# Kernel tuning notes

Hardware: AMD Instinct MI355X
Metric: run time of the kernel (lower is better)

## Reference

```python
import jax, jax.numpy as jnp
import numpy as np

B, H, W, D = 8, 64, 64, 512
NH, DK = 16, 32
WS, SH = 8, 4            # window size, shift size = WS // 2
L = 4                    # n_layer
WS2 = WS * WS
NWH, NWW = H // WS, W // WS
SCALE = 1.0 / np.sqrt(DK)


def _rel_index(ws):
    # standard Swin relative position index: (ws^2, ws^2) into a (2ws-1)^2 table
    coords = np.stack(np.meshgrid(np.arange(ws), np.arange(ws), indexing='ij'))
    cf = coords.reshape(2, -1)
    rel = cf[:, :, None] - cf[:, None, :] + (ws - 1)
    return (rel[0] * (2 * ws - 1) + rel[1]).astype(np.int32)


def _shift_mask():
    # Swin-style shifted-window attention mask for cyclic shift by SH
    img = np.zeros((H, W), dtype=np.int32)
    cnt = 0
    sls = (slice(0, -WS), slice(-WS, -SH), slice(-SH, None))
    for hs in sls:
        for ws_ in sls:
            img[hs, ws_] = cnt
            cnt += 1
    win = img.reshape(NWH, WS, NWW, WS).transpose(0, 2, 1, 3).reshape(NWH, NWW, WS2)
    m = win[..., None, :] != win[..., :, None]          # (nh, nw, ws2, ws2)
    return np.broadcast_to(m[None, None], (1, NH, NWH, NWW, WS2, WS2)).copy()


def setup_inputs() -> dict:
    key = jax.random.key(0)
    ks = jax.random.split(key, 12)
    s = 0.02
    inp = {
        'x': jax.random.normal(ks[0], (B, H, W, D), jnp.float32),
        'mask': jnp.asarray(_shift_mask()),
        'rel_index': jnp.asarray(_rel_index(WS)),
        'Wq': jax.random.normal(ks[1], (L, D, D), jnp.float32) * s,
        'bq': jnp.zeros((L, D), jnp.float32),
        'Wkv': jax.random.normal(ks[2], (L, D, 2 * D), jnp.float32) * s,
        'bkv': jnp.zeros((L, 2 * D), jnp.float32),
        'Wo': jax.random.normal(ks[3], (L, D, D), jnp.float32) * s,
        'bo': jnp.zeros((L, D), jnp.float32),
        'rel_table': jax.random.normal(ks[4], (L, (2 * WS - 1) ** 2, NH), jnp.float32) * s,
        'ln1_g': jnp.ones((L, D), jnp.float32),
        'ln1_b': jnp.zeros((L, D), jnp.float32),
        'ln2_g': jnp.ones((L, D), jnp.float32),
        'ln2_b': jnp.zeros((L, D), jnp.float32),
        'W1': jax.random.normal(ks[5], (L, D, 4 * D), jnp.float32) * s,
        'b1': jnp.zeros((L, 4 * D), jnp.float32),
        'W2': jax.random.normal(ks[6], (L, 4 * D, D), jnp.float32) * s,
        'b2': jnp.zeros((L, D), jnp.float32),
    }
    return inp


def _ln(x, g, b):
    m = jnp.mean(x, -1, keepdims=True)
    v = jnp.mean(jnp.square(x - m), -1, keepdims=True)
    return (x - m) * jax.lax.rsqrt(v + 1e-5) * g + b


def _partition(t):
    # (B,H,W,NH,DK) -> (B,NH,nh,nw,ws^2,DK)
    t = t.reshape(B, NWH, WS, NWW, WS, NH, DK)
    return t.transpose(0, 5, 1, 3, 2, 4, 6).reshape(B, NH, NWH, NWW, WS2, DK)


def _merge(t):
    # (B,NH,nh,nw,ws^2,DK) -> (B,H,W,NH,DK)
    t = t.reshape(B, NH, NWH, NWW, WS, WS, DK).transpose(0, 2, 4, 3, 5, 1, 6)
    return t.reshape(B, H, W, NH, DK)


def _attn(xn, mask, rel_index, Wq, bq, Wkv, bkv, Wo, bo, table):
    q = (xn @ Wq + bq).reshape(B, H, W, NH, DK)
    kv = (xn @ Wkv + bkv).reshape(B, H, W, 2, NH, DK)
    k, v = kv[..., 0, :, :], kv[..., 1, :, :]
    # cyclic shift (shifting=True since n_class=4)
    q = jnp.roll(q, (-SH, -SH), axis=(1, 2))
    k = jnp.roll(k, (-SH, -SH), axis=(1, 2))
    v = jnp.roll(v, (-SH, -SH), axis=(1, 2))
    qw, kw, vw = _partition(q), _partition(k), _partition(v)
    scores = jnp.einsum('bhnmqd,bhnmkd->bhnmqk', qw, kw) * SCALE
    bias = table[rel_index]                      # (ws2, ws2, NH)
    scores = scores + bias.transpose(2, 0, 1)[None, :, None, None]
    scores = jnp.where(mask, -1e9, scores)
    a = jax.nn.softmax(scores, axis=-1)
    o = jnp.einsum('bhnmqk,bhnmkd->bhnmqd', a, vw)
    o = _merge(o)
    o = jnp.roll(o, (SH, SH), axis=(1, 2))       # reverse cyclic shift
    return o.reshape(B, H, W, D) @ Wo + bo


def reference(x, mask, rel_index, Wq, bq, Wkv, bkv, Wo, bo, rel_table,
              ln1_g, ln1_b, ln2_g, ln2_b, W1, b1, W2, b2):
    for i in range(L):
        x = x + _attn(_ln(x, ln1_g[i], ln1_b[i]), mask, rel_index,
                      Wq[i], bq[i], Wkv[i], bkv[i], Wo[i], bo[i], rel_table[i])
        h = _ln(x, ln2_g[i], ln2_b[i])
        x = x + (jax.nn.gelu(h @ W1[i] + b1[i]) @ W2[i] + b2[i])
    return x
```

## Files before the change

### kernel.cpp

```cpp
#include <hip/hip_runtime.h>
#include <hip/hip_bf16.h>

typedef __hip_bfloat16 bf16;
typedef __attribute__((ext_vector_type(8))) short short8;
typedef __attribute__((ext_vector_type(4))) float f32x4;

#define GLDS16(g, l) __builtin_amdgcn_global_load_lds(                              \
    (__attribute__((address_space(1))) const void*)(g),                             \
    (__attribute__((address_space(3))) void*)(l), 16, 0, 0)

#define SCALE_ 0.17677669529663687f

__global__ void detect_k(const unsigned int* __restrict__ ln1g_raw, int* __restrict__ flag)
{
    if (threadIdx.x == 0) *flag = (ln1g_raw[0] == 0x3F803F80u) ? 0 : 1;
}

__global__ __launch_bounds__(256)
void cvt_small_k(const void* __restrict__ src, bf16* __restrict__ dst, const int n,
                 const int* __restrict__ flag)
{
    const int i = blockIdx.x * 256 + threadIdx.x;
    if (i >= n) return;
    const bool f32 = (*flag != 0);
    dst[i] = f32 ? (bf16)((const float*)src)[i] : ((const bf16*)src)[i];
}

__global__ void transpose2_k(const float* __restrict__ inF, const bf16* __restrict__ inB,
                             bf16* __restrict__ out, const int R, const int C,
                             const int* __restrict__ flag)
{
    __shared__ bf16 tile[32][33];
    const bool f32 = (*flag != 0);
    const int c0 = blockIdx.x * 32, r0 = blockIdx.y * 32;
    const int tx = threadIdx.x, ty = threadIdx.y;
#pragma unroll
    for (int k = 0; k < 4; k++) {
        const long idx = (long)(r0 + ty + k * 8) * C + c0 + tx;
        tile[ty + k * 8][tx] = f32 ? (bf16)inF[idx] : inB[idx];
    }
    __syncthreads();
#pragma unroll
    for (int k = 0; k < 4; k++)
        out[(long)(c0 + ty + k * 8) * R + r0 + tx] = tile[tx][ty + k * 8];
}

__device__ __forceinline__ float gelu_f(float v)
{
    const float u = 0.7978845608028654f * (v + 0.044715f * v * v * v);
    const float e = __expf(-2.0f * u);
    return v * __builtin_amdgcn_rcpf(1.0f + e);
}

#define SBAR()   __builtin_amdgcn_s_barrier()
#define SCHED0() __builtin_amdgcn_sched_barrier(0)
#define WLGKM()  { asm volatile("s_waitcnt lgkmcnt(0)"); SCHED0(); }

template <int EPI>
__global__ __launch_bounds__(512, 2)
void gemm256(const bf16* __restrict__ A, const bf16* __restrict__ Bt,
             const bf16* __restrict__ bias0, const bf16* __restrict__ bias1,
             const int split,
             bf16* __restrict__ outb, float* __restrict__ outf,
             float* __restrict__ outf2,
             const int M, const int N, const int K)
{
    __shared__ char smem[131072] __attribute__((aligned(16)));

    const int nT  = N >> 8;
    const int nwg = gridDim.x;
    const int bid = blockIdx.x;
    const int wg = (bid & 7) * (nwg >> 3) + (bid >> 3);
    const int mb = wg / nT;
    const int nb = wg - mb * nT;
    const int m0 = mb << 8, n0 = nb << 8;

    const int tid  = threadIdx.x;
    const int lane = tid & 63;
    const int wave = tid >> 6;
    const int wm = wave >> 2;
    const int wn = wave & 3;
    const int fr  = lane & 15;
    const int oct = lane >> 4;
    const int l8  = lane >> 3;
    const int cx  = (lane & 7) ^ l8;

    const int T = K >> 6;

    const bf16* Asrc = A  + (long)(m0 + wm * 128 + wn * 32 + l8) * K + cx * 8;
    char*       Adst = smem + wm * 16384 + wn * 4096;
    const int h    = wn >> 1;
    const int bsub = wm * 2 + (wn & 1);
    const bf16* Bsrc = Bt + (long)(n0 + h * 128 + bsub * 32 + l8) * K + cx * 8;
    char*       Bdst = smem + 65536 + h * 16384 + bsub * 4096;

#define STAGE_A(kt, p) {                                                   \
        const bf16* s_ = Asrc + (long)(kt) * 64;                           \
        char* d_ = Adst + (p) * 32768;                                     \
        GLDS16(s_,            d_);                                         \
        GLDS16(s_ +  8L * K,  d_ + 1024);                                  \
        GLDS16(s_ + 16L * K,  d_ + 2048);                                  \
        GLDS16(s_ + 24L * K,  d_ + 3072); }
#define STAGE_B(kt, p) {                                                   \
        const bf16* s_ = Bsrc + (long)(kt) * 64;                           \
        char* d_ = Bdst + (p) * 32768;                                     \
        GLDS16(s_,            d_);                                         \
        GLDS16(s_ +  8L * K,  d_ + 1024);                                  \
        GLDS16(s_ + 16L * K,  d_ + 2048);                                  \
        GLDS16(s_ + 24L * K,  d_ + 3072); }

    const int kx0 = (     oct * 16) ^ ((fr & 7) << 4);
    const int kx1 = (64 + oct * 16) ^ ((fr & 7) << 4);
    const int aoff = (wm * 128 + fr) * 128;
    const int boff = 65536 + (wn * 64 + fr) * 128;

    f32x4 acc[8][4];
#pragma unroll
    for (int m = 0; m < 8; m++)
#pragma unroll
        for (int n = 0; n < 4; n++) acc[m][n] = (f32x4){0.f, 0.f, 0.f, 0.f};

    short8 af[4][2], bf[4][2];

    STAGE_B(0, 0); STAGE_A(0, 0);
    STAGE_B(1, 1); STAGE_A(1, 1);
    SCHED0();
    asm volatile("s_waitcnt vmcnt(8)");
    SCHED0();
    SBAR();

    for (int t = 0; t < T; ++t) {
        const int pOff = (t & 1) << 15;

#pragma unroll
        for (int mm = 0; mm < 4; mm++) {
            af[mm][0] = *(const short8*)(smem + pOff + aoff + mm * 2048 + kx0);
            af[mm][1] = *(const short8*)(smem + pOff + aoff + mm * 2048 + kx1);
        }
#pragma unroll
        for (int nn = 0; nn < 2; nn++) {
            bf[nn][0] = *(const short8*)(smem + pOff + boff + nn * 2048 + kx0);
            bf[nn][1] = *(const short8*)(smem + pOff + boff + nn * 2048 + kx1);
        }
        SCHED0();
        SBAR();
        WLGKM();
        __builtin_amdgcn_s_setprio(1);
#pragma unroll
        for (int ks = 0; ks < 2; ks++)
#pragma unroll
            for (int mm = 0; mm < 4; mm++)
#pragma unroll
                for (int nn = 0; nn < 2; nn++)
                    acc[mm][nn] = __builtin_amdgcn_mfma_f32_16x16x32_bf16(
                        bf[nn][ks], af[mm][ks], acc[mm][nn], 0, 0, 0);
        __builtin_amdgcn_s_setprio(0);
        SCHED0();
        SBAR();

#pragma unroll
        for (int nn = 2; nn < 4; nn++) {
            bf[nn][0] = *(const short8*)(smem + pOff + boff + nn * 2048 + kx0);
            bf[nn][1] = *(const short8*)(smem + pOff + boff + nn * 2048 + kx1);
        }
        SCHED0();
        SBAR();
        WLGKM();
        __builtin_amdgcn_s_setprio(1);
#pragma unroll
        for (int ks = 0; ks < 2; ks++)
#pragma unroll
            for (int mm = 0; mm < 4; mm++)
#pragma unroll
                for (int nn = 2; nn < 4; nn++)
                    acc[mm][nn] = __builtin_amdgcn_mfma_f32_16x16x32_bf16(
                        bf[nn][ks], af[mm][ks], acc[mm][nn], 0, 0, 0);
        __builtin_amdgcn_s_setprio(0);
        SCHED0();
        SBAR();

#pragma unroll
        for (int mm = 0; mm < 4; mm++) {
            af[mm][0] = *(const short8*)(smem + pOff + aoff + (4 + mm) * 2048 + kx0);
            af[mm][1] = *(const short8*)(smem + pOff + aoff + (4 + mm) * 2048 + kx1);
        }
        SCHED0();
        if (t < T - 2) STAGE_B(t + 2, (t & 1));
        SCHED0();
        SBAR();
        WLGKM();
        __builtin_amdgcn_s_setprio(1);
#pragma unroll
        for (int ks = 0; ks < 2; ks++)
#pragma unroll
            for (int mm = 0; mm < 4; mm++)
#pragma unroll
                for (int nn = 2; nn < 4; nn++)
                    acc[4 + mm][nn] = __builtin_amdgcn_mfma_f32_16x16x32_bf16(
                        bf[nn][ks], af[mm][ks], acc[4 + mm][nn], 0, 0, 0);
        __builtin_amdgcn_s_setprio(0);
        SCHED0();
        SBAR();

        if (t < T - 2) STAGE_A(t + 2, (t & 1));
        SCHED0();
        __builtin_amdgcn_s_setprio(1);
#pragma unroll
        for (int ks = 0; ks < 2; ks++)
#pragma unroll
            for (int mm = 0; mm < 4; mm++)
#pragma unroll
                for (int nn = 0; nn < 2; nn++)
                    acc[4 + mm][nn] = __builtin_amdgcn_mfma_f32_16x16x32_bf16(
                        bf[nn][ks], af[mm][ks], acc[4 + mm][nn], 0, 0, 0);
        __builtin_amdgcn_s_setprio(0);
        SCHED0();
        if (t < T - 2)       { asm volatile("s_waitcnt vmcnt(8)"); }
        else if (t == T - 2) { asm volatile("s_waitcnt vmcnt(0)"); }
        SCHED0();
        SBAR();
    }
#undef STAGE_A
#undef STAGE_B

    if (EPI >= 2) {
        const int erow = m0 + wm * 128 + fr;
        const int ecol = n0 + wn * 64 + (oct << 2);
#pragma unroll
        for (int nn = 0; nn < 4; nn++) {
            const int col0 = ecol + nn * 16;
            const bf16* bp = (col0 < split) ? (bias0 + col0) : (bias1 + (col0 - split));
            const float bv0 = (float)bp[0], bv1 = (float)bp[1];
            const float bv2 = (float)bp[2], bv3 = (float)bp[3];
#pragma unroll
            for (int mm = 0; mm < 8; mm++) {
                const long base = (long)(erow + mm * 16) * N + col0;
                float4 o = *(const float4*)(outf + base);
                o.x += acc[mm][nn][0] + bv0;
                o.y += acc[mm][nn][1] + bv1;
                o.z += acc[mm][nn][2] + bv2;
                o.w += acc[mm][nn][3] + bv3;
                if (EPI == 2) *(float4*)(outf  + base) = o;
                else          *(float4*)(outf2 + base) = o;
            }
        }
    } else {
        const int col_l = wn * 64 + (oct << 2);
#pragma unroll
        for (int nn = 0; nn < 4; nn++) {
            const int cl = col_l + nn * 16;
            const int cg = n0 + cl;
            const bf16* bp = (cg < split) ? (bias0 + cg) : (bias1 + (cg - split));
            const float bv0 = (float)bp[0], bv1 = (float)bp[1];
            const float bv2 = (float)bp[2], bv3 = (float)bp[3];
#pragma unroll
            for (int mm = 0; mm < 8; mm++) {
                const int row_l = wm * 128 + mm * 16 + fr;
                float v0 = acc[mm][nn][0] + bv0;
                float v1 = acc[mm][nn][1] + bv1;
                float v2 = acc[mm][nn][2] + bv2;
                float v3 = acc[mm][nn][3] + bv3;
                if (EPI == 1) { v0 = gelu_f(v0); v1 = gelu_f(v1); v2 = gelu_f(v2); v3 = gelu_f(v3); }
                union { ushort4 u; bf16 hh[4]; } pk;
                pk.hh[0] = (bf16)v0; pk.hh[1] = (bf16)v1;
                pk.hh[2] = (bf16)v2; pk.hh[3] = (bf16)v3;
                int ad = (row_l << 9) + (cl << 1);
                ad ^= ((row_l & 7) << 4);
                *(ushort4*)(smem + ad) = pk.u;
            }
        }
        asm volatile("s_waitcnt lgkmcnt(0)");
        SBAR();
        const int rgrp = tid >> 5;
        const int chnk = tid & 31;
#pragma unroll
        for (int rr = 0; rr < 16; rr++) {
            const int row_l = rgrp * 16 + rr;
            int ad = (row_l << 9) + (chnk << 4);
            ad ^= ((row_l & 7) << 4);
            const uint4 val = *(const uint4*)(smem + ad);
            *(uint4*)((char*)outb + ((long)(m0 + row_l) * N + n0) * 2 + (chnk << 4)) = val;
        }
    }
}

__global__ __launch_bounds__(256)
void ln_k(const float* __restrict__ x, const bf16* __restrict__ g,
          const bf16* __restrict__ b, bf16* __restrict__ out)
{
    const int token = blockIdx.x * 4 + (threadIdx.x >> 6);
    const int lane  = threadIdx.x & 63;
    const float* xp = x + (long)token * 512 + lane * 8;
    float4 u0 = ((const float4*)xp)[0];
    float4 u1 = ((const float4*)xp)[1];
    float v[8] = {u0.x, u0.y, u0.z, u0.w, u1.x, u1.y, u1.z, u1.w};
    float s = 0.f, ss = 0.f;
#pragma unroll
    for (int e = 0; e < 8; e++) { s += v[e]; ss += v[e] * v[e]; }
#pragma unroll
    for (int off = 1; off < 64; off <<= 1) {
        s  += __shfl_xor(s,  off);
        ss += __shfl_xor(ss, off);
    }
    const float mean = s * (1.0f / 512.0f);
    const float var  = ss * (1.0f / 512.0f) - mean * mean;
    const float rstd = rsqrtf(var + 1e-5f);
    union { uint4 u; bf16 h[8]; } gg, bb, oo;
    gg.u = *(const uint4*)(g + lane * 8);
    bb.u = *(const uint4*)(b + lane * 8);
#pragma unroll
    for (int e = 0; e < 8; e++)
        oo.h[e] = (bf16)((v[e] - mean) * rstd * (float)gg.h[e] + (float)bb.h[e]);
    *(uint4*)(out + (long)token * 512 + lane * 8) = oo.u;
}

__global__ __launch_bounds__(256)
void lnx_k(const void* __restrict__ xin, const bf16* __restrict__ g,
           const bf16* __restrict__ b, float* __restrict__ xf,
           bf16* __restrict__ out, const int* __restrict__ flag)
{
    const int token = blockIdx.x * 4 + (threadIdx.x >> 6);
    const int lane  = threadIdx.x & 63;
    float v[8];
    if (*flag != 0) {
        const float* xp = (const float*)xin + (long)token * 512 + lane * 8;
        float4 u0 = ((const float4*)xp)[0];
        float4 u1 = ((const float4*)xp)[1];
        v[0] = u0.x; v[1] = u0.y; v[2] = u0.z; v[3] = u0.w;
        v[4] = u1.x; v[5] = u1.y; v[6] = u1.z; v[7] = u1.w;
    } else {
        union { uint4 u; bf16 h[8]; } t;
        t.u = *(const uint4*)((const bf16*)xin + (long)token * 512 + lane * 8);
#pragma unroll
        for (int e = 0; e < 8; e++) v[e] = (float)t.h[e];
    }
    float* xo = xf + (long)token * 512 + lane * 8;
    ((float4*)xo)[0] = make_float4(v[0], v[1], v[2], v[3]);
    ((float4*)xo)[1] = make_float4(v[4], v[5], v[6], v[7]);
    float s = 0.f, ss = 0.f;
#pragma unroll
    for (int e = 0; e < 8; e++) { s += v[e]; ss += v[e] * v[e]; }
#pragma unroll
    for (int off = 1; off < 64; off <<= 1) {
        s  += __shfl_xor(s,  off);
        ss += __shfl_xor(ss, off);
    }
    const float mean = s * (1.0f / 512.0f);
    const float var  = ss * (1.0f / 512.0f) - mean * mean;
    const float rstd = rsqrtf(var + 1e-5f);
    union { uint4 u; bf16 h[8]; } gg, bb, oo;
    gg.u = *(const uint4*)(g + lane * 8);
    bb.u = *(const uint4*)(b + lane * 8);
#pragma unroll
    for (int e = 0; e < 8; e++)
        oo.h[e] = (bf16)((v[e] - mean) * rstd * (float)gg.h[e] + (float)bb.h[e]);
    *(uint4*)(out + (long)token * 512 + lane * 8) = oo.u;
}

__global__ __launch_bounds__(64)
void bias_pre_k(const bf16* __restrict__ table, float* __restrict__ biasF)
{
    const int blk = blockIdx.x;
    const int q = blk & 63, n = (blk >> 6) & 15, c = blk >> 10;
    const int j = threadIdx.x;
    const int ri = q >> 3, ci = q & 7, rj = j >> 3, cj = j & 7;
    const float bias = (float)table[((ri - rj + 7) * 15 + (ci - cj + 7)) * 16 + n];
    const int shi = (c & 1) ? (ri < 4 ? 1 : 2) : 0;
    const int shj = (c & 1) ? (rj < 4 ? 1 : 2) : 0;
    const int swi = (c & 2) ? (ci < 4 ? 1 : 2) : 0;
    const int swj = (c & 2) ? (cj < 4 ? 1 : 2) : 0;
    biasF[((long)blk << 6) + j] = ((shi != shj) || (swi != swj)) ? -1.0e9f : bias;
}

__global__ __launch_bounds__(64, 3)
void attn_k2(const bf16* __restrict__ qkv, const float* __restrict__ biasF,
             bf16* __restrict__ out)
{
    __shared__ char lds[12800];
    const int bid = blockIdx.x;
    const int n  = bid & 15;
    const int ww = (bid >> 4) & 7;
    const int wh = (bid >> 7) & 7;
    const int b  = bid >> 10;
    const int lane = threadIdx.x;
    const int fr  = lane & 15;
    const int oct = lane >> 4;
    const int cls = ((wh == 7) ? 1 : 0) | ((ww == 7) ? 2 : 0);

    {
        const int d  = lane & 31;
        const int jh = lane >> 5;
        const long Ce = (((long)b * 64 + wh * 8 + 4) * 64 + (ww * 8 + 4)) * 1536;
        const long hsub = (wh == 7) ? 6291456L : 0L;
        const long wsub = (ww == 7) ? 98304L   : 0L;
        const long vbase = Ce + 1024 + n * 32 + d;
        long rowb[4];
#pragma unroll
        for (int qq = 0; qq < 4; qq++) {
            const int r = jh * 4 + qq;
            rowb[qq] = vbase + (long)r * 98304 - (r >= 4 ? hsub : 0);
        }
        union { ushort us[8]; uint4 u4; } vg[4];
#pragma unroll
        for (int c = 0; c < 32; c++) {
            const int qq = c >> 3, cj = c & 7;
            const long a = rowb[qq] + (long)cj * 1536 - (cj >= 4 ? wsub : 0);
            vg[qq].us[cj] = *(const ushort*)(qkv + a);
        }
#pragma unroll
        for (int qq = 0; qq < 4; qq++)
            *(uint4*)(lds + d * 144 + jh * 64 + qq * 16) = vg[qq].u4;
    }

    long tok[4];
#pragma unroll
    for (int tt = 0; tt < 4; tt++) {
        const int j = fr + 16 * tt;
        const int rj = j >> 3, cj = j & 7;
        const int gh = (wh * 8 + rj + 4) & 63;
        const int gw = (ww * 8 + cj + 4) & 63;
        tok[tt] = ((long)b * 64 + gh) * 64 + gw;
    }

    short8 kf[4];
#pragma unroll
    for (int t = 0; t < 4; t++)
        kf[t] = *(const short8*)(qkv + tok[t] * 1536 + 512 + n * 32 + oct * 8);

    const float* biasW = biasF + (((long)(cls * 16 + n)) << 12);
    float inv[4];
#pragma unroll
    for (int mm = 0; mm < 4; mm++) {
        const short8 qf = *(const short8*)(qkv + tok[mm] * 1536 + n * 32 + oct * 8);
        f32x4 sv[4];
#pragma unroll
        for (int nn = 0; nn < 4; nn++)
            sv[nn] = __builtin_amdgcn_mfma_f32_16x16x32_bf16(
                kf[nn], qf, (f32x4){0.f, 0.f, 0.f, 0.f}, 0, 0, 0);
        float p[16];
        float mx = -3.0e38f;
#pragma unroll
        for (int nn = 0; nn < 4; nn++) {
            const f32x4 bz = *(const f32x4*)(biasW + ((fr + 16 * mm) << 6) + nn * 16 + oct * 4);
#pragma unroll
            for (int r = 0; r < 4; r++) {
                p[nn * 4 + r] = sv[nn][r] * SCALE_ + bz[r];
                mx = fmaxf(mx, p[nn * 4 + r]);
            }
        }
        mx = fmaxf(mx, __shfl_xor(mx, 16));
        mx = fmaxf(mx, __shfl_xor(mx, 32));
        float sum = 0.f;
#pragma unroll
        for (int e = 0; e < 16; e++) { p[e] = __expf(p[e] - mx); sum += p[e]; }
        sum += __shfl_xor(sum, 16);
        sum += __shfl_xor(sum, 32);
        inv[mm] = __builtin_amdgcn_rcpf(sum);

        const int prow = 4608 + ((fr + 16 * mm) << 7);
#pragma unroll
        for (int nn = 0; nn < 4; nn++) {
            union { bf16 h[2]; unsigned u; } lo, hi;
            lo.h[0] = (bf16)p[nn * 4 + 0]; lo.h[1] = (bf16)p[nn * 4 + 1];
            hi.h[0] = (bf16)p[nn * 4 + 2]; hi.h[1] = (bf16)p[nn * 4 + 3];
            uint2 w; w.x = lo.u; w.y = hi.u;
            *(uint2*)(lds + prow + ((nn * 32 + oct * 8) ^ ((fr & 7) << 4))) = w;
        }
    }

    f32x4 oa[4][2];
#pragma unroll
    for (int mm = 0; mm < 4; mm++)
#pragma unroll
        for (int nd = 0; nd < 2; nd++) oa[mm][nd] = (f32x4){0.f, 0.f, 0.f, 0.f};
#pragma unroll
    for (int kc = 0; kc < 2; kc++) {
        const short8 vt0 = *(const short8*)(lds + fr * 144        + kc * 64 + oct * 16);
        const short8 vt1 = *(const short8*)(lds + (fr + 16) * 144 + kc * 64 + oct * 16);
#pragma unroll
        for (int mm = 0; mm < 4; mm++) {
            const short8 pf = *(const short8*)(lds + 4608 + ((fr + 16 * mm) << 7)
                                  + ((kc * 64 + oct * 16) ^ ((fr & 7) << 4)));
            oa[mm][0] = __builtin_amdgcn_mfma_f32_16x16x32_bf16(vt0, pf, oa[mm][0], 0, 0, 0);
            oa[mm][1] = __builtin_amdgcn_mfma_f32_16x16x32_bf16(vt1, pf, oa[mm][1], 0, 0, 0);
        }
    }

#pragma unroll
    for (int mm = 0; mm < 4; mm++) {
        bf16* op = out + tok[mm] * 512 + n * 32 + oct * 4;
#pragma unroll
        for (int nd = 0; nd < 2; nd++) {
            union { ushort4 u; bf16 h[4]; } o4;
#pragma unroll
            for (int r = 0; r < 4; r++) o4.h[r] = (bf16)(oa[mm][nd][r] * inv[mm]);
            *(ushort4*)(op + nd * 16) = o4.u;
        }
    }
}

extern "C" void kernel_launch(void* const* d_in, const int* in_sizes, int n_in,
                              void* d_out, int out_size, void* d_ws, size_t ws_size,
                              hipStream_t stream)
{
    const void* x_in = d_in[0];
    const void* Wq   = d_in[3];
    const void* bq   = d_in[4];
    const void* Wkv  = d_in[5];
    const void* bkv  = d_in[6];
    const void* Wo   = d_in[7];
    const void* bo   = d_in[8];
    const void* rtab = d_in[9];
    const void* ln1g = d_in[10];
    const void* ln1b = d_in[11];
    const void* ln2g = d_in[12];
    const void* ln2b = d_in[13];
    const void* W1   = d_in[14];
    const void* b1   = d_in[15];
    const void* W2   = d_in[16];
    const void* b2   = d_in[17];

    if (ws_size < (size_t)260046848) return;

    char* ws = (char*)d_ws;
    float* bufX   = (float*)(ws);
    bf16*  bufXN  = (bf16*)(ws + 67108864);
    bf16*  bufQKV = (bf16*)(ws + 100663296);
    bf16*  bufMLP = bufQKV;
    bf16*  bufATT = (bf16*)(ws + 201326592);
    bf16*  wT     = (bf16*)(ws + 234881024);
    bf16*  p_b2w  = (bf16*)(ws + 100663296 - 4096);

    int*  flag = (int*)d_out;
    bf16* pp   = (bf16*)((char*)d_out + 256);
    bf16* p_bq   = pp;
    bf16* p_bkv  = pp + 2048;
    bf16* p_bo   = pp + 6144;
    bf16* p_rtab = pp + 8192;
    bf16* p_l1g  = pp + 22592;
    bf16* p_l1b  = pp + 24640;
    bf16* p_l2g  = pp + 26688;
    bf16* p_l2b  = pp + 28736;
    bf16* p_b1   = pp + 30784;
    bf16* p_b2   = pp + 38976;
    float* biasAll = (float*)((char*)d_out + 33554432);

    const long LSTR = 3145728;

    detect_k<<<1, 64, 0, stream>>>((const unsigned int*)ln1g, flag);

    cvt_small_k<<<8,  256, 0, stream>>>(bq,   p_bq,   2048,  flag);
    cvt_small_k<<<16, 256, 0, stream>>>(bkv,  p_bkv,  4096,  flag);
    cvt_small_k<<<8,  256, 0, stream>>>(bo,   p_bo,   2048,  flag);
    cvt_small_k<<<57, 256, 0, stream>>>(rtab, p_rtab, 14400, flag);
    cvt_small_k<<<8,  256, 0, stream>>>(ln1g, p_l1g,  2048,  flag);
    cvt_small_k<<<8,  256, 0, stream>>>(ln1b, p_l1b,  2048,  flag);
    cvt_small_k<<<8,  256, 0, stream>>>(ln2g, p_l2g,  2048,  flag);
    cvt_small_k<<<8,  256, 0, stream>>>(ln2b, p_l2b,  2048,  flag);
    cvt_small_k<<<32, 256, 0, stream>>>(b1,   p_b1,   8192,  flag);
    cvt_small_k<<<8,  256, 0, stream>>>(b2,   p_b2,   2048,  flag);

    for (int i = 0; i < 4; i++)
        bias_pre_k<<<4096, 64, 0, stream>>>(p_rtab + i * 3600, biasAll + (long)i * 262144);

    for (int i = 0; i < 4; i++) {
        bf16* wl = wT + (long)i * LSTR;
        transpose2_k<<<dim3(16,16), dim3(32,8), 0, stream>>>(
            (const float*)Wq  + (long)i*262144,  (const bf16*)Wq  + (long)i*262144,
            wl,           512,  512, flag);
        transpose2_k<<<dim3(32,16), dim3(32,8), 0, stream>>>(
            (const float*)Wkv + (long)i*524288,  (const bf16*)Wkv + (long)i*524288,
            wl + 262144,  512, 1024, flag);
        transpose2_k<<<dim3(16,16), dim3(32,8), 0, stream>>>(
            (const float*)Wo  + (long)i*262144,  (const bf16*)Wo  + (long)i*262144,
            wl + 786432,  512,  512, flag);
        transpose2_k<<<dim3(64,16), dim3(32,8), 0, stream>>>(
            (const float*)W1  + (long)i*1048576, (const bf16*)W1  + (long)i*1048576,
            wl + 1048576, 512, 2048, flag);
        transpose2_k<<<dim3(16,64), dim3(32,8), 0, stream>>>(
            (const float*)W2  + (long)i*1048576, (const bf16*)W2  + (long)i*1048576,
            wl + 2097152, 2048, 512, flag);
    }

    for (int i = 0; i < 4; i++) {
        const bf16* wl = wT + (long)i * LSTR;
        if (i == 0)
            lnx_k<<<8192, 256, 0, stream>>>(x_in, p_l1g, p_l1b, bufX, bufXN, flag);
        else
            ln_k<<<8192, 256, 0, stream>>>(bufX, p_l1g + i*512, p_l1b + i*512, bufXN);
        gemm256<0><<<768, 512, 0, stream>>>(bufXN, wl, p_bq + i*512, p_bkv + i*1024, 512,
                                            bufQKV, nullptr, nullptr, 32768, 1536, 512);
        attn_k2<<<8192, 64, 0, stream>>>(bufQKV, biasAll + (long)i * 262144, bufATT);
        gemm256<2><<<256, 512, 0, stream>>>(bufATT, wl + 786432, p_bo + i*512, p_bo + i*512, 512,
                                            nullptr, bufX, nullptr, 32768, 512, 512);
        ln_k<<<8192, 256, 0, stream>>>(bufX, p_l2g + i*512, p_l2b + i*512, bufXN);
        gemm256<1><<<1024, 512, 0, stream>>>(bufXN, wl + 1048576, p_b1 + i*2048, p_b1 + i*2048, 2048,
                                             bufMLP, nullptr, nullptr, 32768, 2048, 512);
        if (i < 3) {
            gemm256<2><<<256, 512, 0, stream>>>(bufMLP, wl + 2097152, p_b2 + i*512, p_b2 + i*512, 512,
                                                nullptr, bufX, nullptr, 32768, 512, 2048);
        } else {
            cvt_small_k<<<8, 256, 0, stream>>>(b2, p_b2w, 2048, flag);
            gemm256<3><<<256, 512, 0, stream>>>(bufMLP, wl + 2097152, p_b2w + 1536, p_b2w + 1536, 512,
                                                nullptr, bufX, (float*)d_out, 32768, 512, 2048);
        }
    }
}
```

Measured before the change: 1.743 ms.

## Collapse GEMM main loop into two MFMA phases with fewer barriers

The k-loop in the 256x256 GEMM goes from four fine-grained phases, each with its own barrier and interleaved global-to-LDS staging, to two phases. All four B fragments are loaded at once, and both async stages for tile t+2 are issued together after a single barrier at the end of each iteration. This cuts barrier and wait overhead and gives the compiler larger MFMA blocks to schedule. In exchange, global loads no longer overlap with the compute phases, and the extra live fragments raise register pressure.

Result: slower. 1.795 ms (+3.0%).

```diff
diff --git a/kernel.cpp b/kernel.cpp
--- a/kernel.cpp
+++ b/kernel.cpp
@@ -54,7 +54,6 @@
 
 #define SBAR()   __builtin_amdgcn_s_barrier()
 #define SCHED0() __builtin_amdgcn_sched_barrier(0)
-#define WLGKM()  { asm volatile("s_waitcnt lgkmcnt(0)"); SCHED0(); }
 
 template <int EPI>
 __global__ __launch_bounds__(512, 2)
@@ -138,82 +137,43 @@
             af[mm][1] = *(const short8*)(smem + pOff + aoff + mm * 2048 + kx1);
         }
 #pragma unroll
-        for (int nn = 0; nn < 2; nn++) {
+        for (int nn = 0; nn < 4; nn++) {
             bf[nn][0] = *(const short8*)(smem + pOff + boff + nn * 2048 + kx0);
             bf[nn][1] = *(const short8*)(smem + pOff + boff + nn * 2048 + kx1);
         }
+        asm volatile("s_waitcnt lgkmcnt(0)");
         SCHED0();
-        SBAR();
-        WLGKM();
         __builtin_amdgcn_s_setprio(1);
 #pragma unroll
         for (int ks = 0; ks < 2; ks++)
 #pragma unroll
             for (int mm = 0; mm < 4; mm++)
 #pragma unroll
-                for (int nn = 0; nn < 2; nn++)
+                for (int nn = 0; nn < 4; nn++)
                     acc[mm][nn] = __builtin_amdgcn_mfma_f32_16x16x32_bf16(
                         bf[nn][ks], af[mm][ks], acc[mm][nn], 0, 0, 0);
         __builtin_amdgcn_s_setprio(0);
-        SCHED0();
-        SBAR();
-
-#pragma unroll
-        for (int nn = 2; nn < 4; nn++) {
-            bf[nn][0] = *(const short8*)(smem + pOff + boff + nn * 2048 + kx0);
-            bf[nn][1] = *(const short8*)(smem + pOff + boff + nn * 2048 + kx1);
-        }
-        SCHED0();
-        SBAR();
-        WLGKM();
-        __builtin_amdgcn_s_setprio(1);
-#pragma unroll
-        for (int ks = 0; ks < 2; ks++)
-#pragma unroll
-            for (int mm = 0; mm < 4; mm++)
-#pragma unroll
-                for (int nn = 2; nn < 4; nn++)
-                    acc[mm][nn] = __builtin_amdgcn_mfma_f32_16x16x32_bf16(
-                        bf[nn][ks], af[mm][ks], acc[mm][nn], 0, 0, 0);
-        __builtin_amdgcn_s_setprio(0);
-        SCHED0();
-        SBAR();
 
 #pragma unroll
         for (int mm = 0; mm < 4; mm++) {
             af[mm][0] = *(const short8*)(smem + pOff + aoff + (4 + mm) * 2048 + kx0);
             af[mm][1] = *(const short8*)(smem + pOff + aoff + (4 + mm) * 2048 + kx1);
         }
+        asm volatile("s_waitcnt lgkmcnt(0)");
         SCHED0();
-        if (t < T - 2) STAGE_B(t + 2, (t & 1));
-        SCHED0();
-        SBAR();
-        WLGKM();
         __builtin_amdgcn_s_setprio(1);
 #pragma unroll
         for (int ks = 0; ks < 2; ks++)
 #pragma unroll
             for (int mm = 0; mm < 4; mm++)
 #pragma unroll
-                for (int nn = 2; nn < 4; nn++)
+                for (int nn = 0; nn < 4; nn++)
                     acc[4 + mm][nn] = __builtin_amdgcn_mfma_f32_16x16x32_bf16(
                         bf[nn][ks], af[mm][ks], acc[4 + mm][nn], 0, 0, 0);
         __builtin_amdgcn_s_setprio(0);
-        SCHED0();
+
         SBAR();
-
-        if (t < T - 2) STAGE_A(t + 2, (t & 1));
-        SCHED0();
-        __builtin_amdgcn_s_setprio(1);
-#pragma unroll
-        for (int ks = 0; ks < 2; ks++)
-#pragma unroll
-            for (int mm = 0; mm < 4; mm++)
-#pragma unroll
-                for (int nn = 0; nn < 2; nn++)
-                    acc[4 + mm][nn] = __builtin_amdgcn_mfma_f32_16x16x32_bf16(
-                        bf[nn][ks], af[mm][ks], acc[4 + mm][nn], 0, 0, 0);
-        __builtin_amdgcn_s_setprio(0);
+        if (t < T - 2) { STAGE_B(t + 2, (t & 1)); STAGE_A(t + 2, (t & 1)); }
         SCHED0();
         if (t < T - 2)       { asm volatile("s_waitcnt vmcnt(8)"); }
         else if (t == T - 2) { asm volatile("s_waitcnt vmcnt(0)"); }
```
